# Performance work log

Measured on AMD Instinct MI355X. Metric: run time of the kernel, lower is better.

## Reference

```python
import jax, jax.numpy as jnp
import numpy as np

N_NODES = 100000
N_EDGES = 1600000
F_IN = 16      # n_node_features
H = 64         # InnerNet layer_width
EPS = 1e-5     # BatchNorm eps


def _bn(h, g, b, m, v):
    # eval-mode BatchNorm1d with running stats
    return (h - m) * jax.lax.rsqrt(v + EPS) * g + b


def setup_inputs() -> dict:
    key = jax.random.key(0)
    ks = jax.random.split(key, 32)
    inp = {}
    inp["x"] = jax.random.normal(ks[0], (N_NODES, F_IN), jnp.float32)
    inp["edge_index"] = jax.random.randint(ks[1], (2, N_EDGES), 0, N_NODES, dtype=jnp.int32)
    dims_in = [2 * F_IN, H, H]
    k = 2
    for i, din in enumerate(dims_in):
        inp[f"w{i}"] = jax.random.normal(ks[k], (din, H), jnp.float32) * 0.1; k += 1
        inp[f"b{i}"] = jax.random.normal(ks[k], (H,), jnp.float32) * 0.05; k += 1
        inp[f"g{i}"] = jax.random.uniform(ks[k], (H,), jnp.float32, 0.5, 1.5); k += 1
        inp[f"be{i}"] = jax.random.normal(ks[k], (H,), jnp.float32) * 0.05; k += 1
        inp[f"m{i}"] = jax.random.normal(ks[k], (H,), jnp.float32) * 0.1; k += 1
        inp[f"v{i}"] = jax.random.uniform(ks[k], (H,), jnp.float32, 0.5, 1.5); k += 1
    # end layers: Linear(64+16 -> 128) -> ReLU -> Linear(128 -> 1)
    inp["we0"] = jax.random.normal(ks[k], (H + F_IN, 128), jnp.float32) * 0.1; k += 1
    inp["bee0"] = jax.random.normal(ks[k], (128,), jnp.float32) * 0.05; k += 1
    inp["we1"] = jax.random.normal(ks[k], (128, 1), jnp.float32) * 0.1; k += 1
    inp["bee1"] = jax.random.normal(ks[k], (1,), jnp.float32) * 0.05
    return inp


def reference(x, edge_index, w0, b0, g0, be0, m0, v0, w1, b1, g1, be1, m1, v1,
              w2, b2, g2, be2, m2, v2, we0, bee0, we1, bee1):
    src = edge_index[0]  # j
    dst = edge_index[1]  # i (PyG source_to_target)
    x_i = x[dst]
    x_j = x[src]
    h = jnp.concatenate([x_i, x_j - x_i], axis=1)          # [E, 2F]
    h = jax.nn.relu(_bn(h @ w0 + b0, g0, be0, m0, v0))      # [E, H]
    h = jax.nn.relu(_bn(h @ w1 + b1, g1, be1, m1, v1))
    h = jax.nn.relu(_bn(h @ w2 + b2, g2, be2, m2, v2))
    # mean aggregation over incoming edges at target node i
    seg = jax.ops.segment_sum(h, dst, num_segments=N_NODES)  # [N, H]
    cnt = jax.ops.segment_sum(jnp.ones((h.shape[0],), h.dtype), dst, num_segments=N_NODES)
    agg = seg / jnp.maximum(cnt, 1.0)[:, None]
    y = jax.nn.relu(jnp.concatenate([agg, x], axis=1))       # [N, H+F]
    e = y[src] - y[dst]                                       # EdgeOutputer(torch.sub)
    out = jax.nn.sigmoid(jax.nn.relu(e @ we0 + bee0) @ we1 + bee1)  # [E, 1]
    return out
```

## Files before the change

kernel.cpp:

```cpp
#include <hip/hip_runtime.h>

#define E_N 1600000
#define N_N 100000
#define NBKT 391
#define BCAP 5120
#define EPB 4096

#define OFF_B0F  0
#define OFF_B1F  64
#define OFF_B2F  128
#define OFF_FR0  192
#define OFF_FR1  1216
#define OFF_FR2  3264
#define OFF_FE0  5312
#define OFF_YACC 11456
#define OFF_CNT  6411456
#define OFF_BKT  6511456
#define OFF_ASD  6513024
#define OFF_SRCS 9713024
#define OFF_DSTS 11313024
#define OFF_EORG 12913024

#define STR 72
#define OSTR 104

#define WAVE_SYNC() __asm__ volatile("s_waitcnt lgkmcnt(0)" ::: "memory")

typedef __attribute__((ext_vector_type(8))) short bf16x8;
typedef __attribute__((ext_vector_type(4))) float f32x4;

static __device__ __forceinline__ float b2f(unsigned short u) {
  union { unsigned int i; float f; } c; c.i = ((unsigned int)u) << 16; return c.f;
}
static __device__ __forceinline__ float asf(unsigned int u) {
  union { unsigned int i; float f; } c; c.i = u; return c.f;
}
static __device__ __forceinline__ unsigned short f2b(float f) {
  union { float f; unsigned int i; } c; c.f = f;
  unsigned int r = c.i + 0x7FFFu + ((c.i >> 16) & 1u);
  return (unsigned short)(r >> 16);
}
static __device__ __forceinline__ unsigned int pack2(float a, float b) {
  union { float f; unsigned int i; } ca, cb; ca.f = a; cb.f = b;
  return __builtin_amdgcn_perm(cb.i + 0x8000u, ca.i + 0x8000u, 0x07060302u);
}

__global__ void prep_kernel(
    const float* __restrict__ w0, const float* __restrict__ b0, const float* __restrict__ g0,
    const float* __restrict__ be0, const float* __restrict__ m0, const float* __restrict__ v0,
    const float* __restrict__ w1, const float* __restrict__ b1, const float* __restrict__ g1,
    const float* __restrict__ be1, const float* __restrict__ m1, const float* __restrict__ v1,
    const float* __restrict__ w2, const float* __restrict__ b2, const float* __restrict__ g2,
    const float* __restrict__ be2, const float* __restrict__ m2, const float* __restrict__ v2,
    const float* __restrict__ we0, float* __restrict__ ws) {
  __shared__ float s0[64], s1[64], s2[64];
  int t = threadIdx.x;
  if (t < 64) {
    s0[t] = g0[t] * rsqrtf(v0[t] + 1e-5f);
    s1[t] = g1[t] * rsqrtf(v1[t] + 1e-5f);
    s2[t] = g2[t] * rsqrtf(v2[t] + 1e-5f);
    ws[OFF_B0F + t] = (b0[t] - m0[t]) * s0[t] + be0[t];
    ws[OFF_B1F + t] = (b1[t] - m1[t]) * s1[t] + be1[t];
    ws[OFF_B2F + t] = (b2[t] - m2[t]) * s2[t] + be2[t];
  }
  __syncthreads();
  unsigned short* fr0 = (unsigned short*)(ws + OFF_FR0);
  unsigned short* fr1 = (unsigned short*)(ws + OFF_FR1);
  unsigned short* fr2 = (unsigned short*)(ws + OFF_FR2);
  for (int i = t; i < 2048; i += 256) {
    int j = i & 7, lane = (i >> 3) & 63, mt = i >> 9;
    int f = mt * 16 + (lane & 15);
    int k = (lane >> 4) * 8 + j;
    fr0[i] = f2b(w0[k * 64 + f] * s0[f]);
  }
  for (int i = t; i < 4096; i += 256) {
    int j = i & 7, lane = (i >> 3) & 63, tile = i >> 9;
    int mt = tile >> 1, ks = tile & 1;
    int f = mt * 16 + (lane & 15);
    int k = ks * 32 + (lane >> 4) * 8 + j;
    fr1[i] = f2b(w1[k * 64 + f] * s1[f]);
  }
  for (int i = t; i < 4096; i += 256) {
    int j = i & 7, lane = (i >> 3) & 63, tile = i >> 9;
    int mt = tile >> 1, ks = tile & 1;
    int f = mt * 16 + (lane & 15);
    int k = ks * 32 + (lane >> 4) * 8 + j;
    fr2[i] = f2b(w2[k * 64 + f] * s2[f]);
  }
  unsigned short* fe0 = (unsigned short*)(ws + OFF_FE0);
  for (int i = t; i < 12288; i += 256) {
    int j = i & 7, lane = (i >> 3) & 63, tile = i >> 9;
    int mt = tile / 3, ks = tile - mt * 3;
    int h = mt * 16 + (lane & 15);
    int k = ks * 32 + ((lane >> 4) & 3) * 8 + j;
    fe0[i] = (k < 80) ? f2b(we0[k * 128 + h]) : (unsigned short)0;
  }
}

__global__ __launch_bounds__(256) void binA_hist_kernel(const int* __restrict__ ei,
                                                        int* __restrict__ bcnt) {
  __shared__ int lh[NBKT];
  int t = threadIdx.x;
  for (int i = t; i < NBKT; i += 256) lh[i] = 0;
  __syncthreads();
  int e0 = blockIdx.x * EPB + t;
#pragma unroll
  for (int q = 0; q < 16; ++q) {
    int ee = e0 + q * 256;
    if (ee < E_N) atomicAdd(&lh[ei[E_N + ee] >> 8], 1);
  }
  __syncthreads();
  for (int i = t; i < NBKT; i += 256) {
    int v = lh[i];
    if (v) atomicAdd(&bcnt[i], v);
  }
}

__global__ __launch_bounds__(512) void binA_scan_kernel(const int* __restrict__ bcnt,
                                                        int* __restrict__ bbase,
                                                        int* __restrict__ bcur) {
  __shared__ int s[512];
  int t = threadIdx.x;
  int v = (t < NBKT) ? bcnt[t] : 0;
  s[t] = v;
  __syncthreads();
  for (int off = 1; off < 512; off <<= 1) {
    int a = (t >= off) ? s[t - off] : 0;
    __syncthreads();
    s[t] += a;
    __syncthreads();
  }
  if (t < NBKT) {
    int base = s[t] - v;
    bbase[t] = base;
    bcur[t] = base;
  }
}

__global__ __launch_bounds__(256) void binA_scatter_kernel(const int* __restrict__ ei,
                                                           int* __restrict__ bcur,
                                                           uint2* __restrict__ asd) {
  __shared__ int lh[NBKT];
  __shared__ int lbase[NBKT];
  int t = threadIdx.x;
  for (int i = t; i < NBKT; i += 256) lh[i] = 0;
  __syncthreads();
  int e0 = blockIdx.x * EPB + t;
  int s[16], d[16], r[16];
#pragma unroll
  for (int q = 0; q < 16; ++q) {
    int ee = e0 + q * 256;
    if (ee < E_N) {
      s[q] = ei[ee];
      d[q] = ei[E_N + ee];
      r[q] = atomicAdd(&lh[d[q] >> 8], 1);
    } else d[q] = -1;
  }
  __syncthreads();
  for (int i = t; i < NBKT; i += 256) {
    int c = lh[i];
    lbase[i] = c ? atomicAdd(&bcur[i], c) : 0;
  }
  __syncthreads();
#pragma unroll
  for (int q = 0; q < 16; ++q) {
    if (d[q] >= 0) {
      int ee = e0 + q * 256;
      uint2 ent;
      ent.x = (unsigned)s[q];
      ent.y = ((unsigned)ee << 8) | (unsigned)(d[q] & 255);
      asd[lbase[d[q] >> 8] + r[q]] = ent;
    }
  }
}

__global__ __launch_bounds__(1024) void binB_sort_kernel(
    const uint2* __restrict__ asd, const int* __restrict__ bbase,
    const int* __restrict__ bcnt, int* __restrict__ counts,
    int* __restrict__ srcs, int* __restrict__ dsts, int* __restrict__ eorg) {
  __shared__ uint2 ent[BCAP];
  __shared__ int lh[256], lcur[256];
  const int t = threadIdx.x;
  const int bk = blockIdx.x;
  const int base = bbase[bk];
  int cnt = bcnt[bk];
  if (cnt > BCAP) cnt = BCAP;
  if (t < 256) lh[t] = 0;
  __syncthreads();
  for (int i = t; i < cnt; i += 1024) {
    uint2 v = asd[base + i];
    ent[i] = v;
    atomicAdd(&lh[v.y & 255u], 1);
  }
  __syncthreads();
  int v0 = (t < 256) ? lh[t] : 0;
  int acc = v0;
  for (int off = 1; off < 256; off <<= 1) {
    __syncthreads();
    int up = (t < 256 && t >= off) ? lh[t - off] : 0;
    __syncthreads();
    if (t < 256) lh[t] = acc = acc + up;
    __syncthreads();
    acc = (t < 256) ? lh[t] : 0;
  }
  __syncthreads();
  if (t < 256) lcur[t] = acc - v0;
  __syncthreads();
  {
    int nlocal = N_N - bk * 256;
    if (nlocal > 256) nlocal = 256;
    if (t < nlocal) counts[bk * 256 + t] = v0;
  }
  for (int i = t; i < cnt; i += 1024) {
    uint2 v = ent[i];
    unsigned dl = v.y & 255u;
    int rank = atomicAdd(&lcur[dl], 1);
    int pos = base + rank;
    srcs[pos] = (int)v.x;
    dsts[pos] = (bk << 8) | (int)dl;
    eorg[pos] = (int)(v.y >> 8);
  }
}

template <int KS>
static __device__ __forceinline__ void mfma_layer(
    unsigned short* A, const unsigned short* __restrict__ frag,
    const float* __restrict__ bias, int lane) {
  const int m = lane & 15;
  const int quad = lane >> 4;
  bf16x8 wf[4][KS];
#pragma unroll
  for (int mt = 0; mt < 4; ++mt)
#pragma unroll
    for (int ks = 0; ks < KS; ++ks)
      wf[mt][ks] = *(const bf16x8*)(frag + (((mt * KS + ks) * 64) + lane) * 8);
  f32x4 binit[4];
#pragma unroll
  for (int mt = 0; mt < 4; ++mt)
    binit[mt] = *(const f32x4*)(bias + mt * 16 + quad * 4);
  f32x4 acc[4][4];
#pragma unroll
  for (int mt = 0; mt < 4; ++mt)
#pragma unroll
    for (int nt = 0; nt < 4; ++nt) acc[mt][nt] = binit[mt];
#pragma unroll
  for (int nt = 0; nt < 4; ++nt) {
#pragma unroll
    for (int ks = 0; ks < KS; ++ks) {
      bf16x8 bfr = *(const bf16x8*)(A + (nt * 16 + m) * STR + ks * 32 + quad * 8);
#pragma unroll
      for (int mt = 0; mt < 4; ++mt)
        acc[mt][nt] = __builtin_amdgcn_mfma_f32_16x16x32_bf16(wf[mt][ks], bfr, acc[mt][nt], 0, 0, 0);
    }
  }
  WAVE_SYNC();
#pragma unroll
  for (int mt = 0; mt < 4; ++mt) {
#pragma unroll
    for (int nt = 0; nt < 4; ++nt) {
      f32x4 a = acc[mt][nt];
      uint2 p;
      p.x = pack2(fmaxf(a.x, 0.f), fmaxf(a.y, 0.f));
      p.y = pack2(fmaxf(a.z, 0.f), fmaxf(a.w, 0.f));
      *(uint2*)(A + (nt * 16 + m) * STR + mt * 16 + quad * 4) = p;
    }
  }
  WAVE_SYNC();
}

__global__ __launch_bounds__(256) void edge_inner_kernel(
    const float* __restrict__ x, const int* __restrict__ srcs, const int* __restrict__ dsts,
    const float* __restrict__ ws, float* __restrict__ yacc) {
  __shared__ unsigned short act[4][64 * STR];
  const int tid = threadIdx.x;
  const int w = tid >> 6;
  const int lane = tid & 63;
  unsigned short* A = act[w];

  const int pos = blockIdx.x * 256 + tid;
  const int src = srcs[pos];
  const int dst = dsts[pos];
  unsigned long long runmask = __ballot((lane == 0) || (dst != __shfl_up(dst, 1)));

  const float4* x4 = (const float4*)x;
  float4 xi0 = x4[dst * 4 + 0], xi1 = x4[dst * 4 + 1], xi2 = x4[dst * 4 + 2], xi3 = x4[dst * 4 + 3];
  float4 xj0 = x4[src * 4 + 0], xj1 = x4[src * 4 + 1], xj2 = x4[src * 4 + 2], xj3 = x4[src * 4 + 3];
  float vi[16] = {xi0.x, xi0.y, xi0.z, xi0.w, xi1.x, xi1.y, xi1.z, xi1.w,
                  xi2.x, xi2.y, xi2.z, xi2.w, xi3.x, xi3.y, xi3.z, xi3.w};
  float vj[16] = {xj0.x, xj0.y, xj0.z, xj0.w, xj1.x, xj1.y, xj1.z, xj1.w,
                  xj2.x, xj2.y, xj2.z, xj2.w, xj3.x, xj3.y, xj3.z, xj3.w};
  unsigned int* row = (unsigned int*)(A + lane * STR);
#pragma unroll
  for (int q = 0; q < 8; ++q) row[q] = pack2(vi[2 * q], vi[2 * q + 1]);
#pragma unroll
  for (int q = 0; q < 8; ++q)
    row[8 + q] = pack2(vj[2 * q] - vi[2 * q], vj[2 * q + 1] - vi[2 * q + 1]);
  WAVE_SYNC();

  const unsigned short* fr0 = (const unsigned short*)(ws + OFF_FR0);
  const unsigned short* fr1 = (const unsigned short*)(ws + OFF_FR1);
  const unsigned short* fr2 = (const unsigned short*)(ws + OFF_FR2);
  mfma_layer<1>(A, fr0, ws + OFF_B0F, lane);
  mfma_layer<2>(A, fr1, ws + OFF_B1F, lane);
  mfma_layer<2>(A, fr2, ws + OFF_B2F, lane);

  while (runmask) {
    int a = __ffsll(runmask) - 1;
    runmask &= runmask - 1;
    int b = runmask ? (__ffsll(runmask) - 1) : 64;
    float sum = 0.f;
    for (int eo = a; eo < b; ++eo) sum += b2f(A[eo * STR + lane]);
    int d = __shfl(dst, a);
    atomicAdd(&yacc[(size_t)d * 64 + lane], sum);
  }
}

__global__ __launch_bounds__(256) void h_gemm_kernel(
    const float* __restrict__ yacc, const int* __restrict__ counts,
    const float* __restrict__ x, const unsigned short* __restrict__ fe0,
    unsigned short* __restrict__ hout) {
  __shared__ unsigned short Yt[4][64 * OSTR];
  const int tid = threadIdx.x, w = tid >> 6, lane = tid & 63;
  const int quad = lane >> 4, m = lane & 15;
  unsigned short* Aw = Yt[w];
  const int tb = (blockIdx.x * 4 + w) * 64;
  const int node = tb + lane;
  unsigned short* rowp = Aw + lane * OSTR;
  if (node < N_N) {
    float inv = 1.0f / fmaxf((float)counts[node], 1.0f);
    const float4* ya = (const float4*)(yacc + (size_t)node * 64);
#pragma unroll
    for (int q = 0; q < 16; ++q) {
      float4 t = ya[q];
      uint2 p;
      p.x = pack2(fmaxf(t.x * inv, 0.f), fmaxf(t.y * inv, 0.f));
      p.y = pack2(fmaxf(t.z * inv, 0.f), fmaxf(t.w * inv, 0.f));
      *(uint2*)(rowp + q * 4) = p;
    }
    const float4* xx = (const float4*)(x + (size_t)node * 16);
#pragma unroll
    for (int q = 0; q < 4; ++q) {
      float4 t = xx[q];
      uint2 p;
      p.x = pack2(fmaxf(t.x, 0.f), fmaxf(t.y, 0.f));
      p.y = pack2(fmaxf(t.z, 0.f), fmaxf(t.w, 0.f));
      *(uint2*)(rowp + 64 + q * 4) = p;
    }
  } else {
    uint4 z; z.x = z.y = z.z = z.w = 0u;
#pragma unroll
    for (int q = 0; q < 10; ++q) *(uint4*)(rowp + q * 8) = z;
  }
  { uint4 z; z.x = z.y = z.z = z.w = 0u;
    *(uint4*)(rowp + 80) = z; *(uint4*)(rowp + 88) = z; }
  WAVE_SYNC();

  bf16x8 bfr[4][3];
#pragma unroll
  for (int nt = 0; nt < 4; ++nt)
#pragma unroll
    for (int ks = 0; ks < 3; ++ks)
      bfr[nt][ks] = *(const bf16x8*)(Aw + (nt * 16 + m) * OSTR + ks * 32 + quad * 8);

  for (int mt = 0; mt < 8; ++mt) {
    bf16x8 wf[3];
#pragma unroll
    for (int ks = 0; ks < 3; ++ks)
      wf[ks] = *(const bf16x8*)(fe0 + (size_t)(((mt * 3 + ks) * 64) + lane) * 8);
    f32x4 acc[4];
#pragma unroll
    for (int nt = 0; nt < 4; ++nt) { acc[nt].x = 0.f; acc[nt].y = 0.f; acc[nt].z = 0.f; acc[nt].w = 0.f; }
#pragma unroll
    for (int nt = 0; nt < 4; ++nt)
#pragma unroll
      for (int ks = 0; ks < 3; ++ks)
        acc[nt] = __builtin_amdgcn_mfma_f32_16x16x32_bf16(wf[ks], bfr[nt][ks], acc[nt], 0, 0, 0);
#pragma unroll
    for (int nt = 0; nt < 4; ++nt) {
      int n2 = tb + nt * 16 + m;
      if (n2 < N_N) {
        f32x4 a = acc[nt];
        uint2 p;
        p.x = pack2(a.x, a.y);
        p.y = pack2(a.z, a.w);
        *(uint2*)(hout + (size_t)n2 * 128 + mt * 16 + quad * 4) = p;
      }
    }
  }
}

__global__ __launch_bounds__(256) void edge_z_kernel(
    const unsigned short* __restrict__ h,
    const int* __restrict__ srcs, const int* __restrict__ dsts,
    const int* __restrict__ eorg,
    const float* __restrict__ bee0, const float* __restrict__ we1,
    const float* __restrict__ bee1, float* __restrict__ out) {
  const int pos = blockIdx.x * 256 + threadIdx.x;
  const int src = srcs[pos], dst = dsts[pos];
  const uint4* ph_s = (const uint4*)(h + (size_t)src * 128);
  const uint4* ph_d = (const uint4*)(h + (size_t)dst * 128);
  float z0 = 0.f, z1 = 0.f, z2 = 0.f, z3 = 0.f;
#pragma unroll 4
  for (int c = 0; c < 16; ++c) {
    uint4 a = ph_s[c], b = ph_d[c];
    const float4 be_a = *(const float4*)(bee0 + c * 8);
    const float4 be_b = *(const float4*)(bee0 + c * 8 + 4);
    const float4 w_a = *(const float4*)(we1 + c * 8);
    const float4 w_b = *(const float4*)(we1 + c * 8 + 4);
    float v;
    v = fmaxf(asf(a.x << 16) - asf(b.x << 16) + be_a.x, 0.f);          z0 = fmaf(v, w_a.x, z0);
    v = fmaxf(asf(a.x & 0xffff0000u) - asf(b.x & 0xffff0000u) + be_a.y, 0.f); z1 = fmaf(v, w_a.y, z1);
    v = fmaxf(asf(a.y << 16) - asf(b.y << 16) + be_a.z, 0.f);          z2 = fmaf(v, w_a.z, z2);
    v = fmaxf(asf(a.y & 0xffff0000u) - asf(b.y & 0xffff0000u) + be_a.w, 0.f); z3 = fmaf(v, w_a.w, z3);
    v = fmaxf(asf(a.z << 16) - asf(b.z << 16) + be_b.x, 0.f);          z0 = fmaf(v, w_b.x, z0);
    v = fmaxf(asf(a.z & 0xffff0000u) - asf(b.z & 0xffff0000u) + be_b.y, 0.f); z1 = fmaf(v, w_b.y, z1);
    v = fmaxf(asf(a.w << 16) - asf(b.w << 16) + be_b.z, 0.f);          z2 = fmaf(v, w_b.z, z2);
    v = fmaxf(asf(a.w & 0xffff0000u) - asf(b.w & 0xffff0000u) + be_b.w, 0.f); z3 = fmaf(v, w_b.w, z3);
  }
  float z = ((z0 + z1) + (z2 + z3)) + bee1[0];
  out[eorg[pos]] = 1.0f / (1.0f + __expf(-z));
}

extern "C" void kernel_launch(void* const* d_in, const int* in_sizes, int n_in,
                              void* d_out, int out_size, void* d_ws, size_t ws_size,
                              hipStream_t stream) {
  const float* x   = (const float*)d_in[0];
  const int* ei    = (const int*)d_in[1];
  const float* w0  = (const float*)d_in[2];
  const float* b0  = (const float*)d_in[3];
  const float* g0  = (const float*)d_in[4];
  const float* be0 = (const float*)d_in[5];
  const float* m0  = (const float*)d_in[6];
  const float* v0  = (const float*)d_in[7];
  const float* w1  = (const float*)d_in[8];
  const float* b1  = (const float*)d_in[9];
  const float* g1  = (const float*)d_in[10];
  const float* be1 = (const float*)d_in[11];
  const float* m1  = (const float*)d_in[12];
  const float* v1  = (const float*)d_in[13];
  const float* w2  = (const float*)d_in[14];
  const float* b2  = (const float*)d_in[15];
  const float* g2  = (const float*)d_in[16];
  const float* be2 = (const float*)d_in[17];
  const float* m2  = (const float*)d_in[18];
  const float* v2  = (const float*)d_in[19];
  const float* we0 = (const float*)d_in[20];
  const float* bee0= (const float*)d_in[21];
  const float* we1 = (const float*)d_in[22];
  const float* bee1= (const float*)d_in[23];
  float* out = (float*)d_out;
  float* ws  = (float*)d_ws;

  int* counts = (int*)(ws + OFF_CNT);
  int* bcnt   = (int*)(ws + OFF_BKT);
  int* bbase  = bcnt + 512;
  int* bcur   = bcnt + 1024;
  uint2* asd  = (uint2*)(ws + OFF_ASD);
  int* srcs   = (int*)(ws + OFF_SRCS);
  int* dsts   = (int*)(ws + OFF_DSTS);
  int* eorg   = (int*)(ws + OFF_EORG);
  unsigned short* h = (unsigned short*)(ws + OFF_YACC);

  hipMemsetAsync(ws + OFF_YACC, 0, (size_t)N_N * 64 * sizeof(float), stream);
  hipMemsetAsync(bcnt, 0, 512 * sizeof(int), stream);
  prep_kernel<<<1, 256, 0, stream>>>(w0, b0, g0, be0, m0, v0,
                                     w1, b1, g1, be1, m1, v1,
                                     w2, b2, g2, be2, m2, v2, we0, ws);
  binA_hist_kernel<<<(E_N + EPB - 1) / EPB, 256, 0, stream>>>(ei, bcnt);
  binA_scan_kernel<<<1, 512, 0, stream>>>(bcnt, bbase, bcur);
  binA_scatter_kernel<<<(E_N + EPB - 1) / EPB, 256, 0, stream>>>(ei, bcur, asd);
  binB_sort_kernel<<<NBKT, 1024, 0, stream>>>(asd, bbase, bcnt, counts, srcs, dsts, eorg);
  edge_inner_kernel<<<E_N / 256, 256, 0, stream>>>(x, srcs, dsts, ws, ws + OFF_YACC);
  h_gemm_kernel<<<(N_N + 255) / 256, 256, 0, stream>>>(ws + OFF_YACC, counts, x,
                                                       (const unsigned short*)(ws + OFF_FE0), h);
  edge_z_kernel<<<E_N / 256, 256, 0, stream>>>(h, srcs, dsts, eorg, bee0, we1, bee1, out);
}
```

Measured before the change: 370.6 us.

## Replace histogram+scan binning with fixed-capacity buckets and atomic output offsets

Removes the histogram and scan kernels by giving each destination bucket a fixed-capacity slot region (BCAP), so the scatter kernel only needs per-bucket atomic cursors. The sort kernel claims its output range with a global atomic instead of a prefix sum. This makes bucket order in srcs/dsts/eorg nondeterministic, but each bucket's edges stay contiguous and sorted by destination. The yacc memset and the bucket-counter memset are folded into the sort and prep kernels, cutting launches and a full pass over edge_index. Edges beyond BCAP in a bucket are silently dropped, which is safe only while bucket sizes stay under capacity for the input distribution.

```diff
diff --git a/kernel.cpp b/kernel.cpp
--- a/kernel.cpp
+++ b/kernel.cpp
@@ -17,9 +17,9 @@
 #define OFF_CNT  6411456
 #define OFF_BKT  6511456
 #define OFF_ASD  6513024
-#define OFF_SRCS 9713024
-#define OFF_DSTS 11313024
-#define OFF_EORG 12913024
+#define OFF_SRCS 10516864
+#define OFF_DSTS 12116864
+#define OFF_EORG 13716864
 
 #define STR 72
 #define OSTR 104
@@ -55,6 +55,7 @@
     const float* __restrict__ we0, float* __restrict__ ws) {
   __shared__ float s0[64], s1[64], s2[64];
   int t = threadIdx.x;
+  for (int i = t; i < 513; i += 256) ((int*)(ws + OFF_BKT))[i] = 0;
   if (t < 64) {
     s0[t] = g0[t] * rsqrtf(v0[t] + 1e-5f);
     s1[t] = g1[t] * rsqrtf(v1[t] + 1e-5f);
@@ -97,46 +98,6 @@
   }
 }
 
-__global__ __launch_bounds__(256) void binA_hist_kernel(const int* __restrict__ ei,
-                                                        int* __restrict__ bcnt) {
-  __shared__ int lh[NBKT];
-  int t = threadIdx.x;
-  for (int i = t; i < NBKT; i += 256) lh[i] = 0;
-  __syncthreads();
-  int e0 = blockIdx.x * EPB + t;
-#pragma unroll
-  for (int q = 0; q < 16; ++q) {
-    int ee = e0 + q * 256;
-    if (ee < E_N) atomicAdd(&lh[ei[E_N + ee] >> 8], 1);
-  }
-  __syncthreads();
-  for (int i = t; i < NBKT; i += 256) {
-    int v = lh[i];
-    if (v) atomicAdd(&bcnt[i], v);
-  }
-}
-
-__global__ __launch_bounds__(512) void binA_scan_kernel(const int* __restrict__ bcnt,
-                                                        int* __restrict__ bbase,
-                                                        int* __restrict__ bcur) {
-  __shared__ int s[512];
-  int t = threadIdx.x;
-  int v = (t < NBKT) ? bcnt[t] : 0;
-  s[t] = v;
-  __syncthreads();
-  for (int off = 1; off < 512; off <<= 1) {
-    int a = (t >= off) ? s[t - off] : 0;
-    __syncthreads();
-    s[t] += a;
-    __syncthreads();
-  }
-  if (t < NBKT) {
-    int base = s[t] - v;
-    bbase[t] = base;
-    bcur[t] = base;
-  }
-}
-
 __global__ __launch_bounds__(256) void binA_scatter_kernel(const int* __restrict__ ei,
                                                            int* __restrict__ bcur,
                                                            uint2* __restrict__ asd) {
@@ -166,29 +127,43 @@
   for (int q = 0; q < 16; ++q) {
     if (d[q] >= 0) {
       int ee = e0 + q * 256;
-      uint2 ent;
-      ent.x = (unsigned)s[q];
-      ent.y = ((unsigned)ee << 8) | (unsigned)(d[q] & 255);
-      asd[lbase[d[q] >> 8] + r[q]] = ent;
+      int bin = d[q] >> 8;
+      int idx = lbase[bin] + r[q];
+      if (idx < BCAP) {
+        uint2 ent;
+        ent.x = (unsigned)s[q];
+        ent.y = ((unsigned)ee << 8) | (unsigned)(d[q] & 255);
+        asd[(size_t)bin * BCAP + idx] = ent;
+      }
     }
   }
 }
 
 __global__ __launch_bounds__(1024) void binB_sort_kernel(
-    const uint2* __restrict__ asd, const int* __restrict__ bbase,
-    const int* __restrict__ bcnt, int* __restrict__ counts,
+    const uint2* __restrict__ asd, int* __restrict__ bcur, int* __restrict__ gcur,
+    int* __restrict__ counts, float* __restrict__ yacc,
     int* __restrict__ srcs, int* __restrict__ dsts, int* __restrict__ eorg) {
   __shared__ uint2 ent[BCAP];
   __shared__ int lh[256], lcur[256];
+  __shared__ int sobase;
   const int t = threadIdx.x;
   const int bk = blockIdx.x;
-  const int base = bbase[bk];
-  int cnt = bcnt[bk];
+  int cnt = bcur[bk];
   if (cnt > BCAP) cnt = BCAP;
+  if (t == 0) sobase = atomicAdd(gcur, cnt);
+  {
+    int nloc = N_N - bk * 256;
+    if (nloc > 256) nloc = 256;
+    float4* y4 = (float4*)(yacc + (size_t)bk * 256 * 64);
+    int n4 = nloc * 16;
+    float4 z4; z4.x = z4.y = z4.z = z4.w = 0.f;
+    for (int i = t; i < n4; i += 1024) y4[i] = z4;
+  }
   if (t < 256) lh[t] = 0;
   __syncthreads();
+  const size_t ibase = (size_t)bk * BCAP;
   for (int i = t; i < cnt; i += 1024) {
-    uint2 v = asd[base + i];
+    uint2 v = asd[ibase + i];
     ent[i] = v;
     atomicAdd(&lh[v.y & 255u], 1);
   }
@@ -211,11 +186,12 @@
     if (nlocal > 256) nlocal = 256;
     if (t < nlocal) counts[bk * 256 + t] = v0;
   }
+  const int obase = sobase;
   for (int i = t; i < cnt; i += 1024) {
     uint2 v = ent[i];
     unsigned dl = v.y & 255u;
     int rank = atomicAdd(&lcur[dl], 1);
-    int pos = base + rank;
+    int pos = obase + rank;
     srcs[pos] = (int)v.x;
     dsts[pos] = (bk << 8) | (int)dl;
     eorg[pos] = (int)(v.y >> 8);
@@ -452,24 +428,20 @@
   float* ws  = (float*)d_ws;
 
   int* counts = (int*)(ws + OFF_CNT);
-  int* bcnt   = (int*)(ws + OFF_BKT);
-  int* bbase  = bcnt + 512;
-  int* bcur   = bcnt + 1024;
+  int* bcur   = (int*)(ws + OFF_BKT);
+  int* gcur   = bcur + 512;
   uint2* asd  = (uint2*)(ws + OFF_ASD);
   int* srcs   = (int*)(ws + OFF_SRCS);
   int* dsts   = (int*)(ws + OFF_DSTS);
   int* eorg   = (int*)(ws + OFF_EORG);
   unsigned short* h = (unsigned short*)(ws + OFF_YACC);
 
-  hipMemsetAsync(ws + OFF_YACC, 0, (size_t)N_N * 64 * sizeof(float), stream);
-  hipMemsetAsync(bcnt, 0, 512 * sizeof(int), stream);
   prep_kernel<<<1, 256, 0, stream>>>(w0, b0, g0, be0, m0, v0,
                                      w1, b1, g1, be1, m1, v1,
                                      w2, b2, g2, be2, m2, v2, we0, ws);
-  binA_hist_kernel<<<(E_N + EPB - 1) / EPB, 256, 0, stream>>>(ei, bcnt);
-  binA_scan_kernel<<<1, 512, 0, stream>>>(bcnt, bbase, bcur);
   binA_scatter_kernel<<<(E_N + EPB - 1) / EPB, 256, 0, stream>>>(ei, bcur, asd);
-  binB_sort_kernel<<<NBKT, 1024, 0, stream>>>(asd, bbase, bcnt, counts, srcs, dsts, eorg);
+  binB_sort_kernel<<<NBKT, 1024, 0, stream>>>(asd, bcur, gcur, counts, ws + OFF_YACC,
+                                              srcs, dsts, eorg);
   edge_inner_kernel<<<E_N / 256, 256, 0, stream>>>(x, srcs, dsts, ws, ws + OFF_YACC);
   h_gemm_kernel<<<(N_N + 255) / 256, 256, 0, stream>>>(ws + OFF_YACC, counts, x,
                                                        (const unsigned short*)(ws + OFF_FE0), h);
```

Measured after the change: 356.6 us. 1.04x faster.
